# Performance work log

Hardware: AMD Instinct MI355X
Metric: run time of the kernel (lower is better)

Reference implementation:

```python
import jax, jax.numpy as jnp
import numpy as np

N = 50000      # nodes
E = 800000     # edges (avg degree 16)
DIN = 128
H = 128
DOUT = 64


def setup_inputs() -> dict:
    key = jax.random.key(0)
    ks = jax.random.split(key, 8)
    x = jax.random.normal(ks[0], (N, DIN), dtype=jnp.float32)
    edge_index = jax.random.randint(ks[1], (2, E), 0, N, dtype=jnp.int32)
    def glorot(k, fi, fo):
        return jax.random.normal(k, (fi, fo), dtype=jnp.float32) * (1.0 / np.sqrt(fi))
    return {
        "x": x,
        "edge_index": edge_index,
        "W1": glorot(ks[2], DIN, H), "b1": jnp.zeros((H,), jnp.float32),
        "W2": glorot(ks[3], H, H),   "b2": jnp.zeros((H,), jnp.float32),
        "W3": glorot(ks[4], H, DOUT),"b3": jnp.zeros((DOUT,), jnp.float32),
    }


def reference(x, edge_index, W1, b1, W2, b2, W3, b3):
    n = x.shape[0]
    # GCNConv: add self-loops, symmetric degree normalization D^-1/2 (A+I) D^-1/2
    loop = jnp.arange(n, dtype=edge_index.dtype)
    src = jnp.concatenate([edge_index[0], loop])  # [E+N]
    dst = jnp.concatenate([edge_index[1], loop])
    deg = jax.ops.segment_sum(jnp.ones(src.shape, x.dtype), dst, num_segments=n)
    dinv = jnp.where(deg > 0, jax.lax.rsqrt(deg), 0.0)
    norm = dinv[src] * dinv[dst]  # [E+N]

    def conv(h, W, b):
        h = h @ W                                   # [N, out]
        msg = h[src] * norm[:, None]                # gather + scale
        return jax.ops.segment_sum(msg, dst, num_segments=n) + b

    # gelu after every layer except the last (forward breaks before act)
    h = jax.nn.gelu(conv(x, W1, b1), approximate=False)
    h = jax.nn.gelu(conv(h, W2, b2), approximate=False)
    return conv(h, W3, b3)
```

## Files before the change

### kernel.cpp

```cpp
#include <hip/hip_runtime.h>
#include <math.h>

#define NDIN 128
#define NHID 128
#define NDOUT 64

typedef _Float16 half2_t __attribute__((ext_vector_type(2)));
typedef _Float16 half4_t __attribute__((ext_vector_type(4)));

__device__ __forceinline__ float gelu_exact(float x) {
    return 0.5f * x * (1.0f + erff(x * 0.70710678118654752f));
}


__global__ void count_kernel(const int* __restrict__ dst, int* __restrict__ count, int E) {
    int e = blockIdx.x * blockDim.x + threadIdx.x;
    if (e < E) atomicAdd(&count[dst[e]], 1);
}

__global__ __launch_bounds__(256) void reduce_blocks_kernel(
    const int* __restrict__ count, int* __restrict__ blocksum, int n) {
    __shared__ int s[256];
    int i = blockIdx.x * 256 + threadIdx.x;
    s[threadIdx.x] = (i < n) ? count[i] : 0;
    __syncthreads();
    for (int off = 128; off > 0; off >>= 1) {
        if (threadIdx.x < off) s[threadIdx.x] += s[threadIdx.x + off];
        __syncthreads();
    }
    if (threadIdx.x == 0) blocksum[blockIdx.x] = s[0];
}

__global__ __launch_bounds__(256) void scan_partials_kernel(
    const int* __restrict__ blocksum, int* __restrict__ blockoff,
    int* __restrict__ rowptr, int nb, int n) {
    __shared__ int s[256];
    int t = threadIdx.x;
    int v = (t < nb) ? blocksum[t] : 0;
    s[t] = v;
    __syncthreads();
    for (int off = 1; off < 256; off <<= 1) {
        int u = (t >= off) ? s[t - off] : 0;
        __syncthreads();
        s[t] += u;
        __syncthreads();
    }
    if (t < nb) blockoff[t] = s[t] - v;
    if (t == 255) rowptr[n] = s[255];
}

__global__ __launch_bounds__(256) void scan_blocks_kernel(
    const int* __restrict__ count, const int* __restrict__ blockoff,
    int* __restrict__ rowptr, float* __restrict__ dinv, int n) {
    __shared__ int s[256];
    int i = blockIdx.x * 256 + threadIdx.x;
    int v = (i < n) ? count[i] : 0;
    s[threadIdx.x] = v;
    __syncthreads();
    for (int off = 1; off < 256; off <<= 1) {
        int u = (threadIdx.x >= off) ? s[threadIdx.x - off] : 0;
        __syncthreads();
        s[threadIdx.x] += u;
        __syncthreads();
    }
    if (i < n) {
        rowptr[i] = blockoff[blockIdx.x] + s[threadIdx.x] - v;
        dinv[i] = rsqrtf((float)(v + 1));
    }
}

__global__ void fill_kernel(const int* __restrict__ src, const int* __restrict__ dst,
                            const float* __restrict__ dinv, const int* __restrict__ rowptr,
                            int* __restrict__ count, int2* __restrict__ adj, int E) {
    int e = blockIdx.x * blockDim.x + threadIdx.x;
    if (e >= E) return;
    int s = src[e], d = dst[e];
    int slot = atomicSub(&count[d], 1) - 1;
    int p = rowptr[d] + slot;
    adj[p] = make_int2(s, __float_as_int(dinv[s] * dinv[d]));
}


template <int BN, int TN>
__global__ __launch_bounds__(256) void gemm_kernel(
    const float* __restrict__ A, const float* __restrict__ B,
    _Float16* __restrict__ T, int M, int K) {
    __shared__ float lds_a[16][68];
    __shared__ float lds_b[16][BN];
    int tid = threadIdx.x;
    int bm = blockIdx.x * 64;
    int tx = tid & 15;
    int ty = tid >> 4;

    float acc[4][TN] = {};

    for (int k0 = 0; k0 < K; k0 += 16) {
        {
            int r = tid >> 2;
            int kc = (tid & 3) << 2;
            int grow = bm + r;
            float4 av;
            if (grow < M) av = *(const float4*)(A + (size_t)grow * K + k0 + kc);
            else { av.x = av.y = av.z = av.w = 0.f; }
            lds_a[kc + 0][r] = av.x;
            lds_a[kc + 1][r] = av.y;
            lds_a[kc + 2][r] = av.z;
            lds_a[kc + 3][r] = av.w;
        }
        {
            const int nf4 = BN * 16 / 4;
            float4 bv = *((const float4*)(B + (size_t)k0 * BN) + tid);
            *((float4*)&lds_b[0][0] + tid) = bv;
            if (nf4 > 256) {
                float4 bv2 = *((const float4*)(B + (size_t)k0 * BN) + tid + 256);
                *((float4*)&lds_b[0][0] + tid + 256) = bv2;
            }
        }
        __syncthreads();
#pragma unroll
        for (int k = 0; k < 16; k++) {
            float4 a4 = *(const float4*)&lds_a[k][ty << 2];
            float av[4] = {a4.x, a4.y, a4.z, a4.w};
            float bv[TN];
            float4 b4 = *(const float4*)&lds_b[k][tx << 2];
            bv[0] = b4.x; bv[1] = b4.y; bv[2] = b4.z; bv[3] = b4.w;
            if (TN == 8) {
                float4 b42 = *(const float4*)&lds_b[k][64 + (tx << 2)];
                bv[4] = b42.x; bv[5] = b42.y; bv[6] = b42.z; bv[7] = b42.w;
            }
#pragma unroll
            for (int i = 0; i < 4; i++)
#pragma unroll
                for (int j = 0; j < TN; j++)
                    acc[i][j] += av[i] * bv[j];
        }
        __syncthreads();
    }
#pragma unroll
    for (int i = 0; i < 4; i++) {
        int grow = bm + (ty << 2) + i;
        if (grow < M) {
            half4_t o0;
            o0[0] = (_Float16)acc[i][0]; o0[1] = (_Float16)acc[i][1];
            o0[2] = (_Float16)acc[i][2]; o0[3] = (_Float16)acc[i][3];
            *(half4_t*)(T + (size_t)grow * BN + (tx << 2)) = o0;
            if (TN == 8) {
                half4_t o1;
                o1[0] = (_Float16)acc[i][4]; o1[1] = (_Float16)acc[i][5];
                o1[2] = (_Float16)acc[i][6]; o1[3] = (_Float16)acc[i][7];
                *(half4_t*)(T + (size_t)grow * BN + 64 + (tx << 2)) = o1;
            }
        }
    }
}


template <int F, bool DOGELU>
__global__ __launch_bounds__(256) void agg_kernel(
    const _Float16* __restrict__ t, const int* __restrict__ rowptr,
    const int2* __restrict__ adj, const float* __restrict__ dinv,
    const float* __restrict__ bias, float* __restrict__ outp, int n) {
    int node = (int)((blockIdx.x * blockDim.x + threadIdx.x) >> 6);
    int lane = threadIdx.x & 63;
    if (node >= n) return;

    float wself = dinv[node];
    wself *= wself;
    int beg = rowptr[node];
    int end = rowptr[node + 1];

    if (F == 128) {
        const half2_t* t2 = (const half2_t*)t;
        half2_t v = t2[(size_t)node * 64 + lane];
        float accx = wself * (float)v[0], accy = wself * (float)v[1];
        for (int e0 = beg; e0 < end; e0 += 64) {
            int rem = end - e0;
            int j = 0; float w = 0.f;
            if (lane < rem) {
                int2 ed = adj[e0 + lane];
                j = ed.x; w = __int_as_float(ed.y);
            }
            int cnt = rem < 64 ? rem : 64;
            for (int c = 0; c < cnt; c += 16) {
#pragma unroll
                for (int i = 0; i < 16; i++) {
                    int jj = __builtin_amdgcn_readlane(j, c + i);
                    float ww = __int_as_float(
                        __builtin_amdgcn_readlane(__float_as_int(w), c + i));
                    half2_t u = t2[(size_t)jj * 64 + lane];
                    accx += ww * (float)u[0];
                    accy += ww * (float)u[1];
                }
            }
        }
        float2 b = ((const float2*)bias)[lane];
        accx += b.x; accy += b.y;
        if (DOGELU) { accx = gelu_exact(accx); accy = gelu_exact(accy); }
        float2 o; o.x = accx; o.y = accy;
        ((float2*)outp)[(size_t)node * 64 + lane] = o;
    } else {
        float acc = wself * (float)t[(size_t)node * 64 + lane];
        for (int e0 = beg; e0 < end; e0 += 64) {
            int rem = end - e0;
            int j = 0; float w = 0.f;
            if (lane < rem) {
                int2 ed = adj[e0 + lane];
                j = ed.x; w = __int_as_float(ed.y);
            }
            int cnt = rem < 64 ? rem : 64;
            for (int c = 0; c < cnt; c += 16) {
#pragma unroll
                for (int i = 0; i < 16; i++) {
                    int jj = __builtin_amdgcn_readlane(j, c + i);
                    float ww = __int_as_float(
                        __builtin_amdgcn_readlane(__float_as_int(w), c + i));
                    acc += ww * (float)t[(size_t)jj * 64 + lane];
                }
            }
        }
        acc += bias[lane];
        if (DOGELU) acc = gelu_exact(acc);
        outp[(size_t)node * 64 + lane] = acc;
    }
}


extern "C" void kernel_launch(void* const* d_in, const int* in_sizes, int n_in,
                              void* d_out, int out_size, void* d_ws, size_t ws_size,
                              hipStream_t stream) {
    const float* x  = (const float*)d_in[0];
    const int* edge = (const int*)d_in[1];
    const float* W1 = (const float*)d_in[2];
    const float* b1 = (const float*)d_in[3];
    const float* W2 = (const float*)d_in[4];
    const float* b2 = (const float*)d_in[5];
    const float* W3 = (const float*)d_in[6];
    const float* b3 = (const float*)d_in[7];
    float* out = (float*)d_out;

    const int N = in_sizes[0] / NDIN;
    const int E = in_sizes[1] / 2;
    const int* src = edge;
    const int* dst = edge + E;
    const int NB = (N + 255) / 256;

    char* p = (char*)d_ws;
    auto alloc = [&](size_t bytes) {
        char* q = p;
        p += (bytes + 255) & ~(size_t)255;
        return q;
    };
    int*       count    = (int*)alloc((size_t)N * 4);
    int*       rowptr   = (int*)alloc((size_t)(N + 1) * 4);
    int*       blocksum = (int*)alloc((size_t)NB * 4);
    int*       blockoff = (int*)alloc((size_t)NB * 4);
    float*     dinv     = (float*)alloc((size_t)N * 4);
    int2*      adj      = (int2*)alloc((size_t)E * 8);
    _Float16*  tbuf     = (_Float16*)alloc((size_t)N * NHID * 2);
    float*     hbuf     = (float*)alloc((size_t)N * NHID * 4);

    hipMemsetAsync(count, 0, (size_t)N * 4, stream);

    count_kernel<<<(E + 255) / 256, 256, 0, stream>>>(dst, count, E);
    reduce_blocks_kernel<<<NB, 256, 0, stream>>>(count, blocksum, N);
    scan_partials_kernel<<<1, 256, 0, stream>>>(blocksum, blockoff, rowptr, NB, N);
    scan_blocks_kernel<<<NB, 256, 0, stream>>>(count, blockoff, rowptr, dinv, N);
    fill_kernel<<<(E + 255) / 256, 256, 0, stream>>>(src, dst, dinv, rowptr, count,
                                                     adj, E);

    dim3 blk(256);
    int mtiles = (N + 63) / 64;
    int agg_blocks = (N + 3) / 4;

    gemm_kernel<128, 8><<<mtiles, blk, 0, stream>>>(x, W1, tbuf, N, NDIN);
    agg_kernel<128, true><<<agg_blocks, blk, 0, stream>>>(tbuf, rowptr, adj,
                                                          dinv, b1, hbuf, N);
    gemm_kernel<128, 8><<<mtiles, blk, 0, stream>>>(hbuf, W2, tbuf, N, NHID);
    agg_kernel<128, true><<<agg_blocks, blk, 0, stream>>>(tbuf, rowptr, adj,
                                                          dinv, b2, hbuf, N);
    gemm_kernel<64, 4><<<mtiles, blk, 0, stream>>>(hbuf, W3, tbuf, N, NHID);
    agg_kernel<64, false><<<agg_blocks, blk, 0, stream>>>(tbuf, rowptr, adj,
                                                          dinv, b3, out, N);
}
```

Measured before the change: 323.9 us.

## Use MFMA fp16 GEMMs with pre-transposed weights and fp16 hidden activations

```diff
diff --git a/kernel.cpp b/kernel.cpp
--- a/kernel.cpp
+++ b/kernel.cpp
@@ -7,6 +7,8 @@
 
 typedef _Float16 half2_t __attribute__((ext_vector_type(2)));
 typedef _Float16 half4_t __attribute__((ext_vector_type(4)));
+typedef _Float16 half8_t __attribute__((ext_vector_type(8)));
+typedef float    float4v __attribute__((ext_vector_type(4)));
 
 __device__ __forceinline__ float gelu_exact(float x) {
     return 0.5f * x * (1.0f + erff(x * 0.70710678118654752f));
@@ -80,86 +82,100 @@
     adj[p] = make_int2(s, __float_as_int(dinv[s] * dinv[d]));
 }
 
-
-template <int BN, int TN>
-__global__ __launch_bounds__(256) void gemm_kernel(
-    const float* __restrict__ A, const float* __restrict__ B,
-    _Float16* __restrict__ T, int M, int K) {
-    __shared__ float lds_a[16][68];
-    __shared__ float lds_b[16][BN];
+__global__ __launch_bounds__(256) void wtrans_kernel(
+    const float* __restrict__ W, _Float16* __restrict__ Wt, int K, int N) {
+    __shared__ float tile[32][33];
+    int tx = threadIdx.x & 31, ty = threadIdx.x >> 5;
+    for (int i = 0; i < 32; i += 8) {
+        int k = blockIdx.y * 32 + ty + i, n = blockIdx.x * 32 + tx;
+        tile[ty + i][tx] = (k < K && n < N) ? W[(size_t)k * N + n] : 0.f;
+    }
+    __syncthreads();
+    for (int i = 0; i < 32; i += 8) {
+        int n = blockIdx.x * 32 + ty + i, k = blockIdx.y * 32 + tx;
+        if (n < N && k < K) Wt[(size_t)n * K + k] = (_Float16)tile[tx][ty + i];
+    }
+}
+
+
+template <int BN, bool AF16>
+__global__ __launch_bounds__(256) void gemm_mfma(
+    const void* __restrict__ Aptr, const _Float16* __restrict__ Bt,
+    _Float16* __restrict__ T, int M) {
+    __shared__ _Float16 lds_a[64][136];
+    __shared__ _Float16 lds_bt[BN][136];
+    const int K = 128;
     int tid = threadIdx.x;
     int bm = blockIdx.x * 64;
-    int tx = tid & 15;
-    int ty = tid >> 4;
-
-    float acc[4][TN] = {};
-
-    for (int k0 = 0; k0 < K; k0 += 16) {
-        {
-            int r = tid >> 2;
-            int kc = (tid & 3) << 2;
+    int wave = tid >> 6, lane = tid & 63;
+    int m = lane & 15, quad = lane >> 4;
+
+    if (AF16) {
+        const _Float16* A = (const _Float16*)Aptr;
+#pragma unroll
+        for (int j = 0; j < 4; j++) {
+            int c = tid + j * 256;
+            int r = c >> 4, col = (c & 15) << 3;
             int grow = bm + r;
-            float4 av;
-            if (grow < M) av = *(const float4*)(A + (size_t)grow * K + k0 + kc);
-            else { av.x = av.y = av.z = av.w = 0.f; }
-            lds_a[kc + 0][r] = av.x;
-            lds_a[kc + 1][r] = av.y;
-            lds_a[kc + 2][r] = av.z;
-            lds_a[kc + 3][r] = av.w;
-        }
-        {
-            const int nf4 = BN * 16 / 4;
-            float4 bv = *((const float4*)(B + (size_t)k0 * BN) + tid);
-            *((float4*)&lds_b[0][0] + tid) = bv;
-            if (nf4 > 256) {
-                float4 bv2 = *((const float4*)(B + (size_t)k0 * BN) + tid + 256);
-                *((float4*)&lds_b[0][0] + tid + 256) = bv2;
-            }
-        }
-        __syncthreads();
-#pragma unroll
-        for (int k = 0; k < 16; k++) {
-            float4 a4 = *(const float4*)&lds_a[k][ty << 2];
-            float av[4] = {a4.x, a4.y, a4.z, a4.w};
-            float bv[TN];
-            float4 b4 = *(const float4*)&lds_b[k][tx << 2];
-            bv[0] = b4.x; bv[1] = b4.y; bv[2] = b4.z; bv[3] = b4.w;
-            if (TN == 8) {
-                float4 b42 = *(const float4*)&lds_b[k][64 + (tx << 2)];
-                bv[4] = b42.x; bv[5] = b42.y; bv[6] = b42.z; bv[7] = b42.w;
-            }
-#pragma unroll
-            for (int i = 0; i < 4; i++)
-#pragma unroll
-                for (int j = 0; j < TN; j++)
-                    acc[i][j] += av[i] * bv[j];
-        }
-        __syncthreads();
-    }
-#pragma unroll
-    for (int i = 0; i < 4; i++) {
-        int grow = bm + (ty << 2) + i;
-        if (grow < M) {
-            half4_t o0;
-            o0[0] = (_Float16)acc[i][0]; o0[1] = (_Float16)acc[i][1];
-            o0[2] = (_Float16)acc[i][2]; o0[3] = (_Float16)acc[i][3];
-            *(half4_t*)(T + (size_t)grow * BN + (tx << 2)) = o0;
-            if (TN == 8) {
-                half4_t o1;
-                o1[0] = (_Float16)acc[i][4]; o1[1] = (_Float16)acc[i][5];
-                o1[2] = (_Float16)acc[i][6]; o1[3] = (_Float16)acc[i][7];
-                *(half4_t*)(T + (size_t)grow * BN + 64 + (tx << 2)) = o1;
-            }
-        }
-    }
-}
-
-
-template <int F, bool DOGELU>
+            uint4 v = make_uint4(0, 0, 0, 0);
+            if (grow < M) v = *(const uint4*)(A + (size_t)grow * K + col);
+            *(uint4*)&lds_a[r][col] = v;
+        }
+    } else {
+        const float* A = (const float*)Aptr;
+#pragma unroll
+        for (int j = 0; j < 8; j++) {
+            int c = tid + j * 256;
+            int r = c >> 5, col = (c & 31) << 2;
+            int grow = bm + r;
+            float4 v = make_float4(0.f, 0.f, 0.f, 0.f);
+            if (grow < M) v = *(const float4*)(A + (size_t)grow * K + col);
+            half4_t h;
+            h[0] = (_Float16)v.x; h[1] = (_Float16)v.y;
+            h[2] = (_Float16)v.z; h[3] = (_Float16)v.w;
+            *(half4_t*)&lds_a[r][col] = h;
+        }
+    }
+    {
+        const int chunks = BN * K / 8;
+        for (int c = tid; c < chunks; c += 256) {
+            int r = c >> 4, col = (c & 15) << 3;
+            *(uint4*)&lds_bt[r][col] = *(const uint4*)(Bt + (size_t)r * K + col);
+        }
+    }
+    __syncthreads();
+
+    const int NT = BN / 16;
+    float4v acc[NT];
+#pragma unroll
+    for (int nt = 0; nt < NT; nt++) acc[nt] = (float4v){0.f, 0.f, 0.f, 0.f};
+
+    int arow = (wave << 4) + m;
+#pragma unroll
+    for (int kc = 0; kc < K; kc += 32) {
+        half8_t a = *(const half8_t*)&lds_a[arow][kc + quad * 8];
+#pragma unroll
+        for (int nt = 0; nt < NT; nt++) {
+            half8_t b = *(const half8_t*)&lds_bt[nt * 16 + m][kc + quad * 8];
+            acc[nt] = __builtin_amdgcn_mfma_f32_16x16x32_f16(a, b, acc[nt], 0, 0, 0);
+        }
+    }
+#pragma unroll
+    for (int nt = 0; nt < NT; nt++) {
+#pragma unroll
+        for (int r = 0; r < 4; r++) {
+            int grow = bm + (wave << 4) + (quad << 2) + r;
+            if (grow < M) T[(size_t)grow * BN + nt * 16 + m] = (_Float16)acc[nt][r];
+        }
+    }
+}
+
+
+template <int F, bool DOGELU, bool OUTF16>
 __global__ __launch_bounds__(256) void agg_kernel(
     const _Float16* __restrict__ t, const int* __restrict__ rowptr,
     const int2* __restrict__ adj, const float* __restrict__ dinv,
-    const float* __restrict__ bias, float* __restrict__ outp, int n) {
+    const float* __restrict__ bias, void* __restrict__ outp, int n) {
     int node = (int)((blockIdx.x * blockDim.x + threadIdx.x) >> 6);
     int lane = threadIdx.x & 63;
     if (node >= n) return;
@@ -196,8 +212,13 @@
         float2 b = ((const float2*)bias)[lane];
         accx += b.x; accy += b.y;
         if (DOGELU) { accx = gelu_exact(accx); accy = gelu_exact(accy); }
-        float2 o; o.x = accx; o.y = accy;
-        ((float2*)outp)[(size_t)node * 64 + lane] = o;
+        if (OUTF16) {
+            half2_t o; o[0] = (_Float16)accx; o[1] = (_Float16)accy;
+            ((half2_t*)outp)[(size_t)node * 64 + lane] = o;
+        } else {
+            float2 o; o.x = accx; o.y = accy;
+            ((float2*)outp)[(size_t)node * 64 + lane] = o;
+        }
     } else {
         float acc = wself * (float)t[(size_t)node * 64 + lane];
         for (int e0 = beg; e0 < end; e0 += 64) {
@@ -220,7 +241,8 @@
         }
         acc += bias[lane];
         if (DOGELU) acc = gelu_exact(acc);
-        outp[(size_t)node * 64 + lane] = acc;
+        if (OUTF16) ((_Float16*)outp)[(size_t)node * 64 + lane] = (_Float16)acc;
+        else        ((float*)outp)[(size_t)node * 64 + lane] = acc;
     }
 }
 
@@ -256,8 +278,11 @@
     int*       blockoff = (int*)alloc((size_t)NB * 4);
     float*     dinv     = (float*)alloc((size_t)N * 4);
     int2*      adj      = (int2*)alloc((size_t)E * 8);
+    _Float16*  W1t      = (_Float16*)alloc((size_t)NHID * NDIN * 2);
+    _Float16*  W2t      = (_Float16*)alloc((size_t)NHID * NHID * 2);
+    _Float16*  W3t      = (_Float16*)alloc((size_t)NDOUT * NHID * 2);
     _Float16*  tbuf     = (_Float16*)alloc((size_t)N * NHID * 2);
-    float*     hbuf     = (float*)alloc((size_t)N * NHID * 4);
+    _Float16*  hbuf     = (_Float16*)alloc((size_t)N * NHID * 2);
 
     hipMemsetAsync(count, 0, (size_t)N * 4, stream);
 
@@ -267,18 +292,21 @@
     scan_blocks_kernel<<<NB, 256, 0, stream>>>(count, blockoff, rowptr, dinv, N);
     fill_kernel<<<(E + 255) / 256, 256, 0, stream>>>(src, dst, dinv, rowptr, count,
                                                      adj, E);
+    wtrans_kernel<<<dim3(NHID / 32, NDIN / 32), 256, 0, stream>>>(W1, W1t, NDIN, NHID);
+    wtrans_kernel<<<dim3(NHID / 32, NHID / 32), 256, 0, stream>>>(W2, W2t, NHID, NHID);
+    wtrans_kernel<<<dim3(NDOUT / 32, NHID / 32), 256, 0, stream>>>(W3, W3t, NHID, NDOUT);
 
     dim3 blk(256);
     int mtiles = (N + 63) / 64;
     int agg_blocks = (N + 3) / 4;
 
-    gemm_kernel<128, 8><<<mtiles, blk, 0, stream>>>(x, W1, tbuf, N, NDIN);
-    agg_kernel<128, true><<<agg_blocks, blk, 0, stream>>>(tbuf, rowptr, adj,
-                                                          dinv, b1, hbuf, N);
-    gemm_kernel<128, 8><<<mtiles, blk, 0, stream>>>(hbuf, W2, tbuf, N, NHID);
-    agg_kernel<128, true><<<agg_blocks, blk, 0, stream>>>(tbuf, rowptr, adj,
-                                                          dinv, b2, hbuf, N);
-    gemm_kernel<64, 4><<<mtiles, blk, 0, stream>>>(hbuf, W3, tbuf, N, NHID);
-    agg_kernel<64, false><<<agg_blocks, blk, 0, stream>>>(tbuf, rowptr, adj,
-                                                          dinv, b3, out, N);
-}
+    gemm_mfma<128, false><<<mtiles, blk, 0, stream>>>(x, W1t, tbuf, N);
+    agg_kernel<128, true, true><<<agg_blocks, blk, 0, stream>>>(tbuf, rowptr, adj,
+                                                                dinv, b1, hbuf, N);
+    gemm_mfma<128, true><<<mtiles, blk, 0, stream>>>(hbuf, W2t, tbuf, N);
+    agg_kernel<128, true, true><<<agg_blocks, blk, 0, stream>>>(tbuf, rowptr, adj,
+                                                                dinv, b2, hbuf, N);
+    gemm_mfma<64, true><<<mtiles, blk, 0, stream>>>(hbuf, W3t, tbuf, N);
+    agg_kernel<64, false, false><<<agg_blocks, blk, 0, stream>>>(tbuf, rowptr, adj,
+                                                                 dinv, b3, out, N);
+}
```

Result: faster. 292.7 us (-9.6%).
